# Kernel tuning notes

Measured on AMD Instinct MI355X. Metric: run time of the kernel, lower is better.

Reference implementation:

```python
import jax, jax.numpy as jnp
import numpy as np

EPS = 1e-5      # eps used in abs() and log()
BN_EPS = 1e-5   # torch BatchNorm2d default eps


def setup_inputs() -> dict:
    key = jax.random.key(0)
    ks = jax.random.split(key, 5)
    N, C, F, T = 16, 4, 257, 1000
    B, K = 8, 80
    xr = jax.random.normal(ks[0], (N, C, F, T), dtype=jnp.float32)
    xi = jax.random.normal(ks[1], (N, C, F, T), dtype=jnp.float32)
    # per-bin complex beamforming weights: (F, B, C) == Conv1d weight (B*F, 1, C) regrouped
    wr = jax.random.normal(ks[2], (F, B, C), dtype=jnp.float32) * 0.25
    wi = jax.random.normal(ks[3], (F, B, C), dtype=jnp.float32) * 0.25
    # nn.Linear(num_bins, spectra_filters, bias=False) weight: (K, F)
    w_proj = jax.random.normal(ks[4], (K, F), dtype=jnp.float32) * (1.0 / np.sqrt(F))
    gamma = jnp.ones((B,), dtype=jnp.float32)
    beta = jnp.zeros((B,), dtype=jnp.float32)
    return {"xr": xr, "xi": xi, "wr": wr, "wi": wi, "w_proj": w_proj,
            "gamma": gamma, "beta": beta}


def reference(xr, xi, wr, wi, w_proj, gamma, beta):
    # Grouped complex conv1d == per-bin complex beamform across mics:
    # out[n,b,t,f] = sum_c w[f,b,c] * x[n,c,f,t] (complex product)
    br = jnp.einsum('ncft,fbc->nbtf', xr, wr) - jnp.einsum('ncft,fbc->nbtf', xi, wi)
    bi = jnp.einsum('ncft,fbc->nbtf', xi, wr) + jnp.einsum('ncft,fbc->nbtf', xr, wi)
    mag = jnp.sqrt(br * br + bi * bi + EPS)              # (N, B, T, F)
    # Linear(F -> K), ReLU, log
    f = jax.nn.relu(jnp.einsum('nbtf,kf->nbtk', mag, w_proj))
    f = jnp.log(f + EPS)                                  # (N, B, T, K)
    # BatchNorm2d over channel axis B (training-mode batch statistics)
    mean = jnp.mean(f, axis=(0, 2, 3), keepdims=True)
    var = jnp.var(f, axis=(0, 2, 3), keepdims=True)
    f = (f - mean) * jax.lax.rsqrt(var + BN_EPS)
    f = f * gamma[None, :, None, None] + beta[None, :, None, None]
    N, B, T, K = f.shape
    # (N, B, T, K) -> (N, T, B*K)
    return jnp.transpose(f, (0, 2, 1, 3)).reshape(N, T, B * K)
```

## Files before the change

### kernel.cpp

```cpp
#include <hip/hip_runtime.h>
#include <math.h>

#define N_ 16
#define C_ 4
#define F_ 257
#define T_ 1000
#define B_ 8
#define K_ 80
#define BK_ 640
#define TT_ 32
#define NT_ 32
#define NBLK (N_ * NT_)
#define MSTR 260
#define WKS  80

#define WT_OFF   0
#define PART_OFF (128 * 1024)
#define SS_OFF   (PART_OFF + NBLK * 16 * 8)

__global__ __launch_bounds__(80) void k_wt(const float* __restrict__ wp,
                                           float* __restrict__ wT) {
    int f = blockIdx.x;
    int k = threadIdx.x;
    wT[f * WKS + k] = wp[k * F_ + f];
}

__global__ __launch_bounds__(256, 2) void k_fused(
    const float* __restrict__ xr, const float* __restrict__ xi,
    const float* __restrict__ wr, const float* __restrict__ wi,
    const float* __restrict__ wT,
    float* __restrict__ out, double* __restrict__ partials) {

    const int tid = threadIdx.x;
    const int bid = blockIdx.x;
    const int tt = bid & (NT_ - 1);
    const int n  = bid >> 5;
    const int t0 = tt * TT_;

    __shared__ float magS[TT_][MSTR];
    __shared__ double redS1[4][2][4];
    __shared__ double redS2[4][2][4];

    const int t_loc = tid & 31;
    const int bh    = (tid >> 5) & 1;
    const int kg    = __builtin_amdgcn_readfirstlane(tid >> 6);

    const int sfr = tid >> 3;
    const int stq = tid & 7;
    const int tb  = t0 + stq * 4;
    const bool tload = (tb + 4 <= T_);

    float acc[4][20];
#pragma unroll
    for (int jb = 0; jb < 4; ++jb)
#pragma unroll
        for (int j = 0; j < 20; ++j) acc[jb][j] = 0.f;

    const float* xrn = xr + (size_t)n * C_ * F_ * T_;
    const float* xin = xi + (size_t)n * C_ * F_ * T_;

    float4 pxr[C_], pxi[C_];
    if (tload) {
        const float* xrp = xrn + (size_t)sfr * T_ + tb;
        const float* xip = xin + (size_t)sfr * T_ + tb;
#pragma unroll
        for (int c = 0; c < C_; ++c) {
            pxr[c] = *(const float4*)(xrp + (size_t)c * F_ * T_);
            pxi[c] = *(const float4*)(xip + (size_t)c * F_ * T_);
        }
    }

    for (int ch = 0; ch < 8; ++ch) {
        const int f0 = ch * 32;
        const int f  = f0 + sfr;

        __syncthreads();

        {
            float m[4][B_];
            if (tload) {
                float xrv[C_][4], xiv[C_][4];
#pragma unroll
                for (int c = 0; c < C_; ++c) {
                    xrv[c][0] = pxr[c].x; xrv[c][1] = pxr[c].y;
                    xrv[c][2] = pxr[c].z; xrv[c][3] = pxr[c].w;
                    xiv[c][0] = pxi[c].x; xiv[c][1] = pxi[c].y;
                    xiv[c][2] = pxi[c].z; xiv[c][3] = pxi[c].w;
                }
                const float* wrp = wr + (size_t)f * B_ * C_;
                const float* wip = wi + (size_t)f * B_ * C_;
#pragma unroll
                for (int b = 0; b < B_; ++b) {
                    float4 wrv = *(const float4*)(wrp + b * C_);
                    float4 wiv = *(const float4*)(wip + b * C_);
                    float wrc[4] = {wrv.x, wrv.y, wrv.z, wrv.w};
                    float wic[4] = {wiv.x, wiv.y, wiv.z, wiv.w};
#pragma unroll
                    for (int i = 0; i < 4; ++i) {
                        float br = 0.f, bi2 = 0.f;
#pragma unroll
                        for (int c = 0; c < C_; ++c) {
                            br  += xrv[c][i] * wrc[c] - xiv[c][i] * wic[c];
                            bi2 += xiv[c][i] * wrc[c] + xrv[c][i] * wic[c];
                        }
                        m[i][b] = sqrtf(br * br + bi2 * bi2 + 1e-5f);
                    }
                }
            } else {
#pragma unroll
                for (int i = 0; i < 4; ++i)
#pragma unroll
                    for (int b = 0; b < B_; ++b) m[i][b] = 0.f;
            }
#pragma unroll
            for (int i = 0; i < 4; ++i) {
                *(float4*)&magS[stq * 4 + i][sfr * 8] =
                    make_float4(m[i][0], m[i][1], m[i][2], m[i][3]);
                *(float4*)&magS[stq * 4 + i][sfr * 8 + 4] =
                    make_float4(m[i][4], m[i][5], m[i][6], m[i][7]);
            }
        }

        if (ch < 7 && tload) {
            const float* xrp = xrn + (size_t)(f0 + 32 + sfr) * T_ + tb;
            const float* xip = xin + (size_t)(f0 + 32 + sfr) * T_ + tb;
#pragma unroll
            for (int c = 0; c < C_; ++c) {
                pxr[c] = *(const float4*)(xrp + (size_t)c * F_ * T_);
                pxi[c] = *(const float4*)(xip + (size_t)c * F_ * T_);
            }
        }

        __syncthreads();

        const float* wchunk = wT + (size_t)f0 * WKS + kg * 20;
#pragma unroll 2
        for (int fc = 0; fc < 32; ++fc) {
            float4 mv = *(const float4*)&magS[t_loc][fc * 8 + bh * 4];
            float wv[20];
#pragma unroll
            for (int j = 0; j < 20; ++j) wv[j] = wchunk[fc * WKS + j];
            float mbv[4] = {mv.x, mv.y, mv.z, mv.w};
#pragma unroll
            for (int jb = 0; jb < 4; ++jb)
#pragma unroll
                for (int j = 0; j < 20; ++j)
                    acc[jb][j] += mbv[jb] * wv[j];
        }
    }

    __syncthreads();
    {
        int trow = tid >> 3;
        int b = tid & 7;
        int t = t0 + trow;
        float v = 0.f;
        if (t < T_) {
            const float* wrp = wr + (size_t)(256 * B_ + b) * C_;
            const float* wip = wi + (size_t)(256 * B_ + b) * C_;
            float br = 0.f, bi2 = 0.f;
#pragma unroll
            for (int c = 0; c < C_; ++c) {
                float xrv = xrn[((size_t)c * F_ + 256) * T_ + t];
                float xiv = xin[((size_t)c * F_ + 256) * T_ + t];
                br  += xrv * wrp[c] - xiv * wip[c];
                bi2 += xiv * wrp[c] + xrv * wip[c];
            }
            v = sqrtf(br * br + bi2 * bi2 + 1e-5f);
        }
        magS[trow][b] = v;
    }
    __syncthreads();
    {
        float4 mv = *(const float4*)&magS[t_loc][bh * 4];
        const float* wtail = wT + (size_t)256 * WKS + kg * 20;
        float mbv[4] = {mv.x, mv.y, mv.z, mv.w};
#pragma unroll
        for (int jb = 0; jb < 4; ++jb)
#pragma unroll
            for (int j = 0; j < 20; ++j)
                acc[jb][j] += mbv[jb] * wtail[j];
    }

    float s1f[4], s2f[4];
#pragma unroll
    for (int jb = 0; jb < 4; ++jb) { s1f[jb] = 0.f; s2f[jb] = 0.f; }
    const int t = t0 + t_loc;
    if (t < T_) {
        float* obase = out + ((size_t)n * T_ + t) * BK_ + (bh * 4) * K_ + kg * 20;
#pragma unroll
        for (int jb = 0; jb < 4; ++jb) {
            float vv[20];
#pragma unroll
            for (int j = 0; j < 20; ++j) {
                float v = fmaxf(acc[jb][j], 0.0f);
                v = __logf(v + 1e-5f);
                vv[j] = v;
                s1f[jb] += v;
                s2f[jb] += v * v;
            }
            float* orow = obase + jb * K_;
#pragma unroll
            for (int q = 0; q < 5; ++q)
                *(float4*)(orow + q * 4) =
                    make_float4(vv[q * 4], vv[q * 4 + 1], vv[q * 4 + 2], vv[q * 4 + 3]);
        }
    }
    const int wav = tid >> 6;
#pragma unroll
    for (int jb = 0; jb < 4; ++jb) {
        double d1 = (double)s1f[jb], d2 = (double)s2f[jb];
#pragma unroll
        for (int off = 16; off; off >>= 1) {
            d1 += __shfl_xor(d1, off);
            d2 += __shfl_xor(d2, off);
        }
        if ((tid & 31) == 0) { redS1[wav][bh][jb] = d1; redS2[wav][bh][jb] = d2; }
    }
    __syncthreads();
    if (tid < 8) {
        int bh2 = tid >> 2, jb2 = tid & 3;
        partials[(size_t)bid * 16 + tid] =
            redS1[0][bh2][jb2] + redS1[1][bh2][jb2] + redS1[2][bh2][jb2] + redS1[3][bh2][jb2];
    } else if (tid >= 64 && tid < 72) {
        int id = tid - 64;
        int bh2 = id >> 2, jb2 = id & 3;
        partials[(size_t)bid * 16 + 8 + id] =
            redS2[0][bh2][jb2] + redS2[1][bh2][jb2] + redS2[2][bh2][jb2] + redS2[3][bh2][jb2];
    }
}

__global__ __launch_bounds__(256) void k_bnstats(
    const double* __restrict__ partials,
    const float* __restrict__ gamma, const float* __restrict__ beta,
    float* __restrict__ ss) {
    const int b = threadIdx.x >> 5;
    const int i = threadIdx.x & 31;
    double s1 = 0.0, s2 = 0.0;
    for (int j = i; j < NBLK; j += 32) {
        s1 += partials[(size_t)j * 16 + b];
        s2 += partials[(size_t)j * 16 + 8 + b];
    }
#pragma unroll
    for (int off = 16; off; off >>= 1) {
        s1 += __shfl_down(s1, off);
        s2 += __shfl_down(s2, off);
    }
    if (i == 0) {
        const double cnt = (double)N_ * T_ * K_;
        double mean = s1 / cnt;
        double var = s2 / cnt - mean * mean;
        float scale = gamma[b] * (float)(1.0 / sqrt(var + 1e-5));
        float shift = beta[b] - (float)mean * scale;
        ss[b] = scale;
        ss[B_ + b] = shift;
    }
}

__global__ __launch_bounds__(256) void k_bnapply(float* __restrict__ out,
                                                 const float* __restrict__ ss) {
    size_t i4 = (size_t)blockIdx.x * 256 + threadIdx.x;
    int k4 = (int)(i4 % (BK_ / 4));
    int b = k4 / (K_ / 4);
    float scale = ss[b], shift = ss[B_ + b];
    float4* p = (float4*)out + i4;
    float4 v = *p;
    v.x = v.x * scale + shift;
    v.y = v.y * scale + shift;
    v.z = v.z * scale + shift;
    v.w = v.w * scale + shift;
    *p = v;
}

extern "C" void kernel_launch(void* const* d_in, const int* in_sizes, int n_in,
                              void* d_out, int out_size, void* d_ws, size_t ws_size,
                              hipStream_t stream) {
    const float* xr = (const float*)d_in[0];
    const float* xi = (const float*)d_in[1];
    const float* wr = (const float*)d_in[2];
    const float* wi = (const float*)d_in[3];
    const float* w_proj = (const float*)d_in[4];
    const float* gamma = (const float*)d_in[5];
    const float* beta = (const float*)d_in[6];
    float* out = (float*)d_out;

    float* wT = (float*)((char*)d_ws + WT_OFF);
    double* partials = (double*)((char*)d_ws + PART_OFF);
    float* ss = (float*)((char*)d_ws + SS_OFF);

    k_wt<<<F_, 80, 0, stream>>>(w_proj, wT);
    k_fused<<<NBLK, 256, 0, stream>>>(xr, xi, wr, wi, wT, out, partials);
    k_bnstats<<<1, 256, 0, stream>>>(partials, gamma, beta, ss);
    k_bnapply<<<10000, 256, 0, stream>>>(out, ss);
}
```

Before: 157.8 us.

## Halve time tile to 16 per block and double occupancy target

Shrinks each block's time tile from 32 to 16 steps, which doubles the grid to 63 tiles per batch item. Each thread now holds 2x20 accumulators instead of 4x20, and launch bounds request 4 blocks per CU instead of 2. The thread mapping, the reduction shuffles and the partial-stat layout are reworked to match. The aim is more parallelism and better latency hiding; in exchange each block reuses the projection weights over fewer time steps, so weight traffic per output rises.

```diff
diff --git a/kernel.cpp b/kernel.cpp
--- a/kernel.cpp
+++ b/kernel.cpp
@@ -8,10 +8,10 @@
 #define B_ 8
 #define K_ 80
 #define BK_ 640
-#define TT_ 32
-#define NT_ 32
+#define TT_ 16
+#define NT_ 63
 #define NBLK (N_ * NT_)
-#define MSTR 260
+#define MSTR 262
 #define WKS  80
 
 #define WT_OFF   0
@@ -25,7 +25,7 @@
     wT[f * WKS + k] = wp[k * F_ + f];
 }
 
-__global__ __launch_bounds__(256, 2) void k_fused(
+__global__ __launch_bounds__(256, 4) void k_fused(
     const float* __restrict__ xr, const float* __restrict__ xi,
     const float* __restrict__ wr, const float* __restrict__ wi,
     const float* __restrict__ wT,
@@ -33,40 +33,40 @@
 
     const int tid = threadIdx.x;
     const int bid = blockIdx.x;
-    const int tt = bid & (NT_ - 1);
-    const int n  = bid >> 5;
+    const int tt = bid % NT_;
+    const int n  = bid / NT_;
     const int t0 = tt * TT_;
 
     __shared__ float magS[TT_][MSTR];
-    __shared__ double redS1[4][2][4];
-    __shared__ double redS2[4][2][4];
-
-    const int t_loc = tid & 31;
-    const int bh    = (tid >> 5) & 1;
+    __shared__ double redS1[4][4][2];
+    __shared__ double redS2[4][4][2];
+
+    const int t_loc = tid & 15;
+    const int bq    = (tid >> 4) & 3;
     const int kg    = __builtin_amdgcn_readfirstlane(tid >> 6);
 
     const int sfr = tid >> 3;
-    const int stq = tid & 7;
-    const int tb  = t0 + stq * 4;
-    const bool tload = (tb + 4 <= T_);
-
-    float acc[4][20];
-#pragma unroll
-    for (int jb = 0; jb < 4; ++jb)
-#pragma unroll
-        for (int j = 0; j < 20; ++j) acc[jb][j] = 0.f;
+    const int st2 = tid & 7;
+    const int tb  = t0 + st2 * 2;
+    const bool tload = (tb + 2 <= T_);
+
+    float acc[2][20];
+#pragma unroll
+    for (int i = 0; i < 2; ++i)
+#pragma unroll
+        for (int j = 0; j < 20; ++j) acc[i][j] = 0.f;
 
     const float* xrn = xr + (size_t)n * C_ * F_ * T_;
     const float* xin = xi + (size_t)n * C_ * F_ * T_;
 
-    float4 pxr[C_], pxi[C_];
+    float2 pxr[C_], pxi[C_];
     if (tload) {
         const float* xrp = xrn + (size_t)sfr * T_ + tb;
         const float* xip = xin + (size_t)sfr * T_ + tb;
 #pragma unroll
         for (int c = 0; c < C_; ++c) {
-            pxr[c] = *(const float4*)(xrp + (size_t)c * F_ * T_);
-            pxi[c] = *(const float4*)(xip + (size_t)c * F_ * T_);
+            pxr[c] = *(const float2*)(xrp + (size_t)c * F_ * T_);
+            pxi[c] = *(const float2*)(xip + (size_t)c * F_ * T_);
         }
     }
 
@@ -77,15 +77,13 @@
         __syncthreads();
 
         {
-            float m[4][B_];
+            float m[2][B_];
             if (tload) {
-                float xrv[C_][4], xiv[C_][4];
+                float xrv[C_][2], xiv[C_][2];
 #pragma unroll
                 for (int c = 0; c < C_; ++c) {
                     xrv[c][0] = pxr[c].x; xrv[c][1] = pxr[c].y;
-                    xrv[c][2] = pxr[c].z; xrv[c][3] = pxr[c].w;
                     xiv[c][0] = pxi[c].x; xiv[c][1] = pxi[c].y;
-                    xiv[c][2] = pxi[c].z; xiv[c][3] = pxi[c].w;
                 }
                 const float* wrp = wr + (size_t)f * B_ * C_;
                 const float* wip = wi + (size_t)f * B_ * C_;
@@ -96,7 +94,7 @@
                     float wrc[4] = {wrv.x, wrv.y, wrv.z, wrv.w};
                     float wic[4] = {wiv.x, wiv.y, wiv.z, wiv.w};
 #pragma unroll
-                    for (int i = 0; i < 4; ++i) {
+                    for (int i = 0; i < 2; ++i) {
                         float br = 0.f, bi2 = 0.f;
 #pragma unroll
                         for (int c = 0; c < C_; ++c) {
@@ -108,15 +106,15 @@
                 }
             } else {
 #pragma unroll
-                for (int i = 0; i < 4; ++i)
+                for (int i = 0; i < 2; ++i)
 #pragma unroll
                     for (int b = 0; b < B_; ++b) m[i][b] = 0.f;
             }
 #pragma unroll
-            for (int i = 0; i < 4; ++i) {
-                *(float4*)&magS[stq * 4 + i][sfr * 8] =
+            for (int i = 0; i < 2; ++i) {
+                *(float4*)&magS[st2 * 2 + i][sfr * 8] =
                     make_float4(m[i][0], m[i][1], m[i][2], m[i][3]);
-                *(float4*)&magS[stq * 4 + i][sfr * 8 + 4] =
+                *(float4*)&magS[st2 * 2 + i][sfr * 8 + 4] =
                     make_float4(m[i][4], m[i][5], m[i][6], m[i][7]);
             }
         }
@@ -126,31 +124,30 @@
             const float* xip = xin + (size_t)(f0 + 32 + sfr) * T_ + tb;
 #pragma unroll
             for (int c = 0; c < C_; ++c) {
-                pxr[c] = *(const float4*)(xrp + (size_t)c * F_ * T_);
-                pxi[c] = *(const float4*)(xip + (size_t)c * F_ * T_);
+                pxr[c] = *(const float2*)(xrp + (size_t)c * F_ * T_);
+                pxi[c] = *(const float2*)(xip + (size_t)c * F_ * T_);
             }
         }
 
         __syncthreads();
 
         const float* wchunk = wT + (size_t)f0 * WKS + kg * 20;
-#pragma unroll 2
+#pragma unroll 4
         for (int fc = 0; fc < 32; ++fc) {
-            float4 mv = *(const float4*)&magS[t_loc][fc * 8 + bh * 4];
+            float2 mv = *(const float2*)&magS[t_loc][fc * 8 + bq * 2];
             float wv[20];
 #pragma unroll
             for (int j = 0; j < 20; ++j) wv[j] = wchunk[fc * WKS + j];
-            float mbv[4] = {mv.x, mv.y, mv.z, mv.w};
-#pragma unroll
-            for (int jb = 0; jb < 4; ++jb)
-#pragma unroll
-                for (int j = 0; j < 20; ++j)
-                    acc[jb][j] += mbv[jb] * wv[j];
+#pragma unroll
+            for (int j = 0; j < 20; ++j) {
+                acc[0][j] += mv.x * wv[j];
+                acc[1][j] += mv.y * wv[j];
+            }
         }
     }
 
     __syncthreads();
-    {
+    if (tid < 128) {
         int trow = tid >> 3;
         int b = tid & 7;
         int t = t0 + trow;
@@ -172,34 +169,33 @@
     }
     __syncthreads();
     {
-        float4 mv = *(const float4*)&magS[t_loc][bh * 4];
+        float2 mv = *(const float2*)&magS[t_loc][bq * 2];
         const float* wtail = wT + (size_t)256 * WKS + kg * 20;
-        float mbv[4] = {mv.x, mv.y, mv.z, mv.w};
-#pragma unroll
-        for (int jb = 0; jb < 4; ++jb)
-#pragma unroll
-            for (int j = 0; j < 20; ++j)
-                acc[jb][j] += mbv[jb] * wtail[j];
-    }
-
-    float s1f[4], s2f[4];
-#pragma unroll
-    for (int jb = 0; jb < 4; ++jb) { s1f[jb] = 0.f; s2f[jb] = 0.f; }
+#pragma unroll
+        for (int j = 0; j < 20; ++j) {
+            float wv = wtail[j];
+            acc[0][j] += mv.x * wv;
+            acc[1][j] += mv.y * wv;
+        }
+    }
+
+    float s1f[2], s2f[2];
+    s1f[0] = s1f[1] = s2f[0] = s2f[1] = 0.f;
     const int t = t0 + t_loc;
     if (t < T_) {
-        float* obase = out + ((size_t)n * T_ + t) * BK_ + (bh * 4) * K_ + kg * 20;
-#pragma unroll
-        for (int jb = 0; jb < 4; ++jb) {
+        float* obase = out + ((size_t)n * T_ + t) * BK_ + (bq * 2) * K_ + kg * 20;
+#pragma unroll
+        for (int i = 0; i < 2; ++i) {
             float vv[20];
 #pragma unroll
             for (int j = 0; j < 20; ++j) {
-                float v = fmaxf(acc[jb][j], 0.0f);
+                float v = fmaxf(acc[i][j], 0.0f);
                 v = __logf(v + 1e-5f);
                 vv[j] = v;
-                s1f[jb] += v;
-                s2f[jb] += v * v;
-            }
-            float* orow = obase + jb * K_;
+                s1f[i] += v;
+                s2f[i] += v * v;
+            }
+            float* orow = obase + i * K_;
 #pragma unroll
             for (int q = 0; q < 5; ++q)
                 *(float4*)(orow + q * 4) =
@@ -208,25 +204,25 @@
     }
     const int wav = tid >> 6;
 #pragma unroll
-    for (int jb = 0; jb < 4; ++jb) {
-        double d1 = (double)s1f[jb], d2 = (double)s2f[jb];
-#pragma unroll
-        for (int off = 16; off; off >>= 1) {
+    for (int i = 0; i < 2; ++i) {
+        double d1 = (double)s1f[i], d2 = (double)s2f[i];
+#pragma unroll
+        for (int off = 1; off < 16; off <<= 1) {
             d1 += __shfl_xor(d1, off);
             d2 += __shfl_xor(d2, off);
         }
-        if ((tid & 31) == 0) { redS1[wav][bh][jb] = d1; redS2[wav][bh][jb] = d2; }
+        if (t_loc == 0) { redS1[wav][bq][i] = d1; redS2[wav][bq][i] = d2; }
     }
     __syncthreads();
     if (tid < 8) {
-        int bh2 = tid >> 2, jb2 = tid & 3;
+        int bqi = tid >> 1, ii = tid & 1;
         partials[(size_t)bid * 16 + tid] =
-            redS1[0][bh2][jb2] + redS1[1][bh2][jb2] + redS1[2][bh2][jb2] + redS1[3][bh2][jb2];
+            redS1[0][bqi][ii] + redS1[1][bqi][ii] + redS1[2][bqi][ii] + redS1[3][bqi][ii];
     } else if (tid >= 64 && tid < 72) {
         int id = tid - 64;
-        int bh2 = id >> 2, jb2 = id & 3;
+        int bqi = id >> 1, ii = id & 1;
         partials[(size_t)bid * 16 + 8 + id] =
-            redS2[0][bh2][jb2] + redS2[1][bh2][jb2] + redS2[2][bh2][jb2] + redS2[3][bh2][jb2];
+            redS2[0][bqi][ii] + redS2[1][bqi][ii] + redS2[2][bqi][ii] + redS2[3][bqi][ii];
     }
 }
 
```

Result: slower. 179.7 us (+13.9%).
